# Optimization experiments

Measured on AMD Instinct MI355X. Metric: run time of the kernel, lower is better.

Reference implementation:

```python
import jax, jax.numpy as jnp
import numpy as np

TEMPERATURE = 0.07
EPS = 1e-12  # matches torch F.normalize default eps


def setup_inputs() -> dict:
    key = jax.random.key(0)
    k1, k2 = jax.random.split(key)
    features1 = jax.random.normal(k1, (16384, 512), dtype=jnp.float32)
    features2 = jax.random.normal(k2, (16384, 512), dtype=jnp.float32)
    return {"features1": features1, "features2": features2}


def _l2_normalize(x):
    # torch F.normalize: x / max(||x||, eps)
    norm = jnp.sqrt(jnp.sum(x * x, axis=1, keepdims=True))
    return x / jnp.maximum(norm, EPS)


def reference(features1, features2):
    f1 = _l2_normalize(features1)
    f2 = _l2_normalize(features2)
    # [N, N] similarity logits
    logits = jnp.einsum('nd,md->nm', f1, f2) / TEMPERATURE
    n = logits.shape[0]
    # cross-entropy with labels = arange(n): mean over rows of (logsumexp - diag logit)
    log_probs = jax.nn.log_softmax(logits, axis=1)
    diag = jnp.diagonal(log_probs)
    loss = -jnp.mean(diag)
    return loss
```

## Files before the change

kernel.cpp:

```cpp
#include <hip/hip_runtime.h>
#include <stdint.h>

#define NROWS 16384
#define KDIM  512
#define BM 256
#define BN 128
#define CT 4
#define NCHUNK 32
#define NPH 16
#define INV_T 14.285714285714286f
#define LOG2E 1.4426950408889634f
#define LN2   0.6931471805599453f

typedef __bf16 bf16x8 __attribute__((ext_vector_type(8)));
typedef float  f32x16 __attribute__((ext_vector_type(16)));
typedef unsigned short u16x8 __attribute__((ext_vector_type(8)));

__device__ __forceinline__ void gload_lds16(const void* gptr, void* lptr) {
    uint32_t loff = (uint32_t)(uintptr_t)lptr;
    loff = __builtin_amdgcn_readfirstlane(loff);
    __builtin_amdgcn_global_load_lds(
        (const uint32_t __attribute__((address_space(1)))*)(uintptr_t)gptr,
        (uint32_t __attribute__((address_space(3)))*)(uintptr_t)loff,
        16, 0, 0);
}


__global__ void k_norm(const float* __restrict__ X, char* __restrict__ Y, float scale) {
    const int row  = blockIdx.x * 4 + (threadIdx.x >> 6);
    const int lane = threadIdx.x & 63;
    const float* xr = X + (size_t)row * KDIM + lane * 8;
    float4 a = *(const float4*)xr;
    float4 b = *(const float4*)(xr + 4);
    float ss = a.x*a.x + a.y*a.y + a.z*a.z + a.w*a.w
             + b.x*b.x + b.y*b.y + b.z*b.z + b.w*b.w;
    #pragma unroll
    for (int off = 1; off < 64; off <<= 1) ss += __shfl_xor(ss, off);
    const float s = scale / fmaxf(sqrtf(ss), 1e-12f);
    __bf16 o[8];
    o[0] = (__bf16)(a.x * s); o[1] = (__bf16)(a.y * s);
    o[2] = (__bf16)(a.z * s); o[3] = (__bf16)(a.w * s);
    o[4] = (__bf16)(b.x * s); o[5] = (__bf16)(b.y * s);
    o[6] = (__bf16)(b.z * s); o[7] = (__bf16)(b.w * s);
    const int kh = lane >> 2, q = lane & 3;
    const size_t gr = ((size_t)(kh * 512 + (row >> 5)) * 2 + (q >> 1)) * 64
                    + ((q & 1) << 5) + (row & 31);
    *(u16x8*)(Y + gr * 16) = *(const u16x8*)o;
}

__global__ __launch_bounds__(512, 2) void k_gemm(const char* __restrict__ A,
                                                 const char* __restrict__ B,
                                                 float* __restrict__ S_part) {
    __shared__ __align__(16) char L[4 * 24576];
    __shared__ float rowsum[2][BM];
    char* Lc = (char*)L;

    const int tid  = threadIdx.x;
    const int lane = tid & 63;
    const int w    = tid >> 6;
    const int wr   = w >> 1, wc = w & 1;
    const int bid  = blockIdx.x;
    const int xcd  = bid & 7;
    const int idx  = bid >> 3;
    const int st   = idx >> 5;
    const int wsub = idx & 31;
    const int sg   = xcd * 8 + st;
    const int bg   = sg & 7, cg = sg >> 3;
    const int brow  = (bg * 8 + (wsub >> 2)) * BM;
    const int chunk = cg * 4 + (wsub & 3);
    const int rbA0 = brow >> 5;

#define STGA(KH_, S_) do {                                                    \
        const char* g_ = A + ((size_t)((KH_) * 512 + rbA0) * 2048) + tid * 16;\
        char* l_ = Lc + (S_) * 24576 + tid * 16;                              \
        gload_lds16(g_,        l_);                                           \
        gload_lds16(g_ + 8192, l_ + 8192);                                    \
    } while (0)

#define STGB(KH_, S_) do {                                                    \
        const char* g_ = B + ((size_t)((KH_) * 512 + rbB0) * 2048) + tid * 16;\
        char* l_ = Lc + (S_) * 24576 + 16384 + tid * 16;                      \
        gload_lds16(g_, l_);                                                  \
    } while (0)

    float rowacc = 0.f;
    #pragma unroll 1
    for (int ct = 0; ct < CT; ++ct) {
        const int rbB0 = (chunk * 16 + ct * 4);
        f32x16 acc[2][2] = {};
        bf16x8 af[2][2], bf[2][2];

        STGA(0, 0); STGB(0, 0);
        STGA(1, 1); STGB(1, 1);
        asm volatile("s_waitcnt vmcnt(3)" ::: "memory");
        __builtin_amdgcn_s_barrier();

        #pragma unroll
        for (int h = 0; h < NPH; ++h) {
            const char* sl = Lc + (h & 3) * 24576;
            #pragma unroll
            for (int m = 0; m < 2; ++m)
                #pragma unroll
                for (int ks = 0; ks < 2; ++ks)
                    af[m][ks] = *(const bf16x8*)(sl + ((wr * 2 + m) << 11)
                                                 + (ks << 10) + (lane << 4));
            #pragma unroll
            for (int n = 0; n < 2; ++n)
                #pragma unroll
                for (int ks = 0; ks < 2; ++ks)
                    bf[n][ks] = *(const bf16x8*)(sl + 16384 + ((wc * 2 + n) << 11)
                                                 + (ks << 10) + (lane << 4));
            if (h < NPH - 2) { STGA(h + 2, (h + 2) & 3); STGB(h + 2, (h + 2) & 3); }
            __builtin_amdgcn_sched_barrier(0);
            if (h < NPH - 2)       asm volatile("s_waitcnt vmcnt(3)" ::: "memory");
            else if (h == NPH - 2) asm volatile("s_waitcnt vmcnt(0)" ::: "memory");
            __builtin_amdgcn_s_barrier();
            asm volatile("s_waitcnt lgkmcnt(0)" ::: "memory");
            __builtin_amdgcn_sched_barrier(0);
            __builtin_amdgcn_s_setprio(1);
            #pragma unroll
            for (int m = 0; m < 2; ++m)
                #pragma unroll
                for (int n = 0; n < 2; ++n)
                    #pragma unroll
                    for (int ks = 0; ks < 2; ++ks)
                        acc[m][n] = __builtin_amdgcn_mfma_f32_32x32x16_bf16(
                            af[m][ks], bf[n][ks], acc[m][n], 0, 0, 0);
            __builtin_amdgcn_s_setprio(0);
            __builtin_amdgcn_s_barrier();
        }

        #pragma unroll
        for (int m = 0; m < 2; ++m) {
            float rs[16];
            #pragma unroll
            for (int r = 0; r < 16; ++r)
                rs[r] = __builtin_amdgcn_exp2f(acc[m][0][r])
                      + __builtin_amdgcn_exp2f(acc[m][1][r]);
            #pragma unroll
            for (int off = 16; off >= 1; off >>= 1)
                #pragma unroll
                for (int r = 0; r < 16; ++r)
                    rs[r] += __shfl_xor(rs[r], off);
            if ((lane & 31) == 0) {
                const int rb = wr * 64 + m * 32 + (lane >> 5) * 4;
                #pragma unroll
                for (int r = 0; r < 16; ++r)
                    rowsum[wc][rb + (r & 3) + 8 * (r >> 2)] = rs[r];
            }
        }
        __syncthreads();
        if (tid < BM) rowacc += rowsum[0][tid] + rowsum[1][tid];
        __syncthreads();
    }
#undef STGA
#undef STGB
    if (tid < BM) S_part[(size_t)chunk * NROWS + brow + tid] = rowacc;
}

__global__ void k_diag(const char* __restrict__ A, const char* __restrict__ B,
                       float* __restrict__ diag) {
    const int row  = blockIdx.x * 4 + (threadIdx.x >> 6);
    const int lane = threadIdx.x & 63;
    const int kh = lane >> 2, q = lane & 3;
    const size_t gr = ((size_t)(kh * 512 + (row >> 5)) * 2 + (q >> 1)) * 64
                    + ((q & 1) << 5) + (row & 31);
    const bf16x8 va = *(const bf16x8*)(A + gr * 16);
    const bf16x8 vb = *(const bf16x8*)(B + gr * 16);
    float d = 0.f;
    #pragma unroll
    for (int i = 0; i < 8; ++i) d += (float)va[i] * (float)vb[i];
    #pragma unroll
    for (int off2 = 1; off2 < 64; off2 <<= 1) d += __shfl_xor(d, off2);
    if (lane == 0) diag[row] = d;
}

__global__ void k_loss(const float* __restrict__ S_part, const float* __restrict__ diag,
                       float* __restrict__ partial) {
    const int g = blockIdx.x * 256 + threadIdx.x;
    float S = 0.f;
    #pragma unroll
    for (int c = 0; c < NCHUNK; ++c) S += S_part[(size_t)c * NROWS + g];
    float v = logf(S) - diag[g] * LN2;
    __shared__ float wsum[4];
    #pragma unroll
    for (int off = 1; off < 64; off <<= 1) v += __shfl_xor(v, off);
    if ((threadIdx.x & 63) == 0) wsum[threadIdx.x >> 6] = v;
    __syncthreads();
    if (threadIdx.x == 0) partial[blockIdx.x] = wsum[0] + wsum[1] + wsum[2] + wsum[3];
}

__global__ void k_final(const float* __restrict__ partial, float* __restrict__ out) {
    float v = partial[threadIdx.x];
    #pragma unroll
    for (int off = 1; off < 64; off <<= 1) v += __shfl_xor(v, off);
    if (threadIdx.x == 0) out[0] = v * (1.0f / (float)NROWS);
}

extern "C" void kernel_launch(void* const* d_in, const int* in_sizes, int n_in,
                              void* d_out, int out_size, void* d_ws, size_t ws_size,
                              hipStream_t stream) {
    const float* f1 = (const float*)d_in[0];
    const float* f2 = (const float*)d_in[1];
    float* out = (float*)d_out;

    char* ws = (char*)d_ws;
    char*  f1p   = ws;
    char*  f2p   = ws + (16u << 20);
    float* S_part = (float*)(ws + (32u << 20));
    float* diag   = (float*)(ws + (34u << 20));
    float* part   = (float*)(ws + (34u << 20) + (1u << 16));

    k_norm<<<dim3(NROWS / 4), dim3(256), 0, stream>>>(f1, f1p, INV_T * LOG2E);
    k_norm<<<dim3(NROWS / 4), dim3(256), 0, stream>>>(f2, f2p, 1.0f);
    k_gemm<<<dim3((NROWS / BM) * NCHUNK), dim3(512), 0, stream>>>(f1p, f2p, S_part);
    k_diag<<<dim3(NROWS / 4), dim3(256), 0, stream>>>(f1p, f2p, diag);
    k_loss<<<dim3(NROWS / 256), dim3(256), 0, stream>>>(S_part, diag, part);
    k_final<<<dim3(1), dim3(64), 0, stream>>>(part, out);
}
```

Before: 370.5 us.

## Double-buffer LDS fragments in registers and deepen global prefetch to three stages

The GEMM main loop now loads the next k-phase's A/B fragments from LDS into a second register set while the MFMAs for the current phase run. This removes the per-iteration lgkmcnt wait and one of the two barriers. Global-to-LDS prefetch distance grows from two to three of the four LDS buffers. Launch bounds drop to one block per CU, which frees registers for the extra fragment set; LDS usage already limited residency to about one block, so little occupancy should be lost. The risk is higher register pressure and tighter reuse of the four LDS stages.

```diff
diff --git a/kernel.cpp b/kernel.cpp
--- a/kernel.cpp
+++ b/kernel.cpp
@@ -48,7 +48,7 @@
     *(u16x8*)(Y + gr * 16) = *(const u16x8*)o;
 }
 
-__global__ __launch_bounds__(512, 2) void k_gemm(const char* __restrict__ A,
+__global__ __launch_bounds__(512, 1) void k_gemm(const char* __restrict__ A,
                                                  const char* __restrict__ B,
                                                  float* __restrict__ S_part) {
     __shared__ __align__(16) char L[4 * 24576];
@@ -83,50 +83,49 @@
         gload_lds16(g_, l_);                                                  \
     } while (0)
 
+#define RDS(SET_, HH_) do {                                                   \
+        const char* sl_ = Lc + ((HH_) & 3) * 24576;                           \
+        _Pragma("unroll") for (int m_ = 0; m_ < 2; ++m_)                      \
+        _Pragma("unroll") for (int ks_ = 0; ks_ < 2; ++ks_)                   \
+            af[SET_][m_][ks_] = *(const bf16x8*)(sl_ + ((wr * 2 + m_) << 11)  \
+                                           + (ks_ << 10) + (lane << 4));      \
+        _Pragma("unroll") for (int n_ = 0; n_ < 2; ++n_)                      \
+        _Pragma("unroll") for (int ks_ = 0; ks_ < 2; ++ks_)                   \
+            bf[SET_][n_][ks_] = *(const bf16x8*)(sl_ + 16384                  \
+                  + ((wc * 2 + n_) << 11) + (ks_ << 10) + (lane << 4));       \
+    } while (0)
+
+#define MM(SET_) do {                                                         \
+        __builtin_amdgcn_s_setprio(1);                                        \
+        _Pragma("unroll") for (int m_ = 0; m_ < 2; ++m_)                      \
+        _Pragma("unroll") for (int n_ = 0; n_ < 2; ++n_)                      \
+        _Pragma("unroll") for (int ks_ = 0; ks_ < 2; ++ks_)                   \
+            acc[m_][n_] = __builtin_amdgcn_mfma_f32_32x32x16_bf16(            \
+                af[SET_][m_][ks_], bf[SET_][n_][ks_], acc[m_][n_], 0, 0, 0);  \
+        __builtin_amdgcn_s_setprio(0);                                        \
+    } while (0)
+
     float rowacc = 0.f;
     #pragma unroll 1
     for (int ct = 0; ct < CT; ++ct) {
         const int rbB0 = (chunk * 16 + ct * 4);
         f32x16 acc[2][2] = {};
-        bf16x8 af[2][2], bf[2][2];
+        bf16x8 af[2][2][2], bf[2][2][2];
 
         STGA(0, 0); STGB(0, 0);
         STGA(1, 1); STGB(1, 1);
+        STGA(2, 2); STGB(2, 2);
         asm volatile("s_waitcnt vmcnt(3)" ::: "memory");
         __builtin_amdgcn_s_barrier();
+        RDS(0, 0);
 
         #pragma unroll
         for (int h = 0; h < NPH; ++h) {
-            const char* sl = Lc + (h & 3) * 24576;
-            #pragma unroll
-            for (int m = 0; m < 2; ++m)
-                #pragma unroll
-                for (int ks = 0; ks < 2; ++ks)
-                    af[m][ks] = *(const bf16x8*)(sl + ((wr * 2 + m) << 11)
-                                                 + (ks << 10) + (lane << 4));
-            #pragma unroll
-            for (int n = 0; n < 2; ++n)
-                #pragma unroll
-                for (int ks = 0; ks < 2; ++ks)
-                    bf[n][ks] = *(const bf16x8*)(sl + 16384 + ((wc * 2 + n) << 11)
-                                                 + (ks << 10) + (lane << 4));
-            if (h < NPH - 2) { STGA(h + 2, (h + 2) & 3); STGB(h + 2, (h + 2) & 3); }
-            __builtin_amdgcn_sched_barrier(0);
-            if (h < NPH - 2)       asm volatile("s_waitcnt vmcnt(3)" ::: "memory");
-            else if (h == NPH - 2) asm volatile("s_waitcnt vmcnt(0)" ::: "memory");
-            __builtin_amdgcn_s_barrier();
-            asm volatile("s_waitcnt lgkmcnt(0)" ::: "memory");
-            __builtin_amdgcn_sched_barrier(0);
-            __builtin_amdgcn_s_setprio(1);
-            #pragma unroll
-            for (int m = 0; m < 2; ++m)
-                #pragma unroll
-                for (int n = 0; n < 2; ++n)
-                    #pragma unroll
-                    for (int ks = 0; ks < 2; ++ks)
-                        acc[m][n] = __builtin_amdgcn_mfma_f32_32x32x16_bf16(
-                            af[m][ks], bf[n][ks], acc[m][n], 0, 0, 0);
-            __builtin_amdgcn_s_setprio(0);
+            if (h < NPH - 1) RDS((h + 1) & 1, h + 1);
+            if (h < NPH - 3) { STGA(h + 3, (h + 3) & 3); STGB(h + 3, (h + 3) & 3); }
+            MM(h & 1);
+            if (h < NPH - 3)       asm volatile("s_waitcnt vmcnt(3)" ::: "memory");
+            else if (h == NPH - 3) asm volatile("s_waitcnt vmcnt(0)" ::: "memory");
             __builtin_amdgcn_s_barrier();
         }
 
@@ -155,6 +154,8 @@
     }
 #undef STGA
 #undef STGB
+#undef RDS
+#undef MM
     if (tid < BM) S_part[(size_t)chunk * NROWS + brow + tid] = rowacc;
 }
 
```

Measured after the change: 358.4 us. 1.03x faster.
